# Performance work log

Hardware: AMD Instinct MI355X
Metric: run time of the kernel (lower is better)

Reference implementation:

```python
import jax, jax.numpy as jnp
import numpy as np

CLASS_NUM = 64
CENTROID_MARGIN = 1.4
EPS = 1e-6
N, D = 262144, 128


def setup_inputs() -> dict:
    key = jax.random.key(0)
    k1, k2 = jax.random.split(key)
    embeddings = jax.random.normal(k1, (N, D), dtype=jnp.float32)
    target = jax.random.randint(k2, (N,), 0, CLASS_NUM, dtype=jnp.int32)
    return {"embeddings": embeddings, "target": target}


def reference(embeddings, target):
    C = CLASS_NUM
    dt = embeddings.dtype
    # per-class sums and counts (equivalent to one-hot broadcast-multiply-sum in the original)
    counts = jax.ops.segment_sum(jnp.ones((embeddings.shape[0],), dtype=dt), target, num_segments=C)  # [C]
    sums = jax.ops.segment_sum(embeddings, target, num_segments=C)  # [C, D]
    class_centers = sums / (counts[:, None] + EPS)  # [C, D]
    # pairwise squared distances between centers
    diff = class_centers[:, None, :] - class_centers[None, :, :]  # [C, C, D]
    cc = jnp.sum(diff * diff, axis=2)  # [C, C]
    cc = jax.nn.relu(CENTROID_MARGIN - jnp.sqrt(cc + EPS)) ** 2
    cc = jnp.triu(cc, k=1).sum() / C * (C - 1) / 2
    # L2 distance of each embedding to its class center
    dist = embeddings - class_centers[target]  # [N, D]
    l2 = jnp.sum(dist * dist, axis=1).mean()
    return l2 + cc
```

## Files before the change

kernel.cpp:

```cpp
#include <hip/hip_runtime.h>

#define CLS 64
#define DIM 128
#define NROWS 262144
#define MARGIN 1.4f
#define EPSF 1e-6f
#define FIXSCALE 1048576.0f
#define INVFIX (1.0f / 1048576.0f)
#define SQSCALE 1048576.0
#define INVSQ (1.0 / 1048576.0)
#define NB 256

__global__ __launch_bounds__(256) void zeroK(int* __restrict__ p, int n) {
    int i = blockIdx.x * 256 + threadIdx.x;
    if (i < n) p[i] = 0;
}

__global__ __launch_bounds__(512, 2) void phaseA(const float* __restrict__ emb,
                                                 const int* __restrict__ tgt,
                                                 int* __restrict__ fsum_i,
                                                 int* __restrict__ fcnt_i,
                                                 unsigned long long* __restrict__ sq64,
                                                 int rowsPerBlock) {
    __shared__ int acc[CLS * DIM];
    __shared__ int cnt[CLS];
    __shared__ float red[8];
    const int tid = threadIdx.x;

    for (int i = tid; i < CLS * DIM; i += 512) acc[i] = 0;
    if (tid < CLS) cnt[tid] = 0;
    __syncthreads();

    const int dl = tid & 31;
    const int rl = tid >> 5;
    const int rowBase = blockIdx.x * rowsPerBlock;
    const int iters = rowsPerBlock >> 6;
    int r = rowBase + rl;

    const float4* __restrict__ embv = reinterpret_cast<const float4*>(emb);

    float4 v0 = embv[(size_t)(r)      * 32 + dl];
    float4 v1 = embv[(size_t)(r + 16) * 32 + dl];
    float4 v2 = embv[(size_t)(r + 32) * 32 + dl];
    float4 v3 = embv[(size_t)(r + 48) * 32 + dl];
    int c0 = tgt[r];
    int c1 = tgt[r + 16];
    int c2 = tgt[r + 32];
    int c3 = tgt[r + 48];

    float sq = 0.f;
    for (int it = 0; it < iters; ++it) {
        float4 x0 = v0, x1 = v1, x2 = v2, x3 = v3;
        int k0 = c0, k1 = c1, k2 = c2, k3 = c3;
        int rn = r + 64;
        if (it + 1 < iters) {
            v0 = embv[(size_t)(rn)      * 32 + dl];
            v1 = embv[(size_t)(rn + 16) * 32 + dl];
            v2 = embv[(size_t)(rn + 32) * 32 + dl];
            v3 = embv[(size_t)(rn + 48) * 32 + dl];
            c0 = tgt[rn];
            c1 = tgt[rn + 16];
            c2 = tgt[rn + 32];
            c3 = tgt[rn + 48];
        }
        r = rn;

        sq += x0.x * x0.x + x0.y * x0.y + x0.z * x0.z + x0.w * x0.w;
        sq += x1.x * x1.x + x1.y * x1.y + x1.z * x1.z + x1.w * x1.w;
        sq += x2.x * x2.x + x2.y * x2.y + x2.z * x2.z + x2.w * x2.w;
        sq += x3.x * x3.x + x3.y * x3.y + x3.z * x3.z + x3.w * x3.w;

        int* row0 = &acc[k0 * DIM];
        atomicAdd(&row0[dl],      __float2int_rn(x0.x * FIXSCALE));
        atomicAdd(&row0[32 + dl], __float2int_rn(x0.y * FIXSCALE));
        atomicAdd(&row0[64 + dl], __float2int_rn(x0.z * FIXSCALE));
        atomicAdd(&row0[96 + dl], __float2int_rn(x0.w * FIXSCALE));
        int* row1 = &acc[k1 * DIM];
        atomicAdd(&row1[dl],      __float2int_rn(x1.x * FIXSCALE));
        atomicAdd(&row1[32 + dl], __float2int_rn(x1.y * FIXSCALE));
        atomicAdd(&row1[64 + dl], __float2int_rn(x1.z * FIXSCALE));
        atomicAdd(&row1[96 + dl], __float2int_rn(x1.w * FIXSCALE));
        int* row2 = &acc[k2 * DIM];
        atomicAdd(&row2[dl],      __float2int_rn(x2.x * FIXSCALE));
        atomicAdd(&row2[32 + dl], __float2int_rn(x2.y * FIXSCALE));
        atomicAdd(&row2[64 + dl], __float2int_rn(x2.z * FIXSCALE));
        atomicAdd(&row2[96 + dl], __float2int_rn(x2.w * FIXSCALE));
        int* row3 = &acc[k3 * DIM];
        atomicAdd(&row3[dl],      __float2int_rn(x3.x * FIXSCALE));
        atomicAdd(&row3[32 + dl], __float2int_rn(x3.y * FIXSCALE));
        atomicAdd(&row3[64 + dl], __float2int_rn(x3.z * FIXSCALE));
        atomicAdd(&row3[96 + dl], __float2int_rn(x3.w * FIXSCALE));
        if (dl == 0) {
            atomicAdd(&cnt[k0], 1);
            atomicAdd(&cnt[k1], 1);
            atomicAdd(&cnt[k2], 1);
            atomicAdd(&cnt[k3], 1);
        }
    }

    for (int o = 32; o > 0; o >>= 1) sq += __shfl_down(sq, o, 64);
    if ((tid & 63) == 0) red[tid >> 6] = sq;
    __syncthreads();

    for (int i = tid; i < CLS * DIM; i += 512) atomicAdd(&fsum_i[i], acc[i]);
    if (tid < CLS) atomicAdd(&fcnt_i[tid], cnt[tid]);
    if (tid == 0) {
        double s = 0.0;
        for (int k = 0; k < 8; ++k) s += (double)red[k];
        atomicAdd(sq64, (unsigned long long)(s * SQSCALE + 0.5));
    }
}

__device__ double blockReduceD(double v, double* scratch, int tid) {
    for (int o = 32; o > 0; o >>= 1) v += __shfl_down(v, o, 64);
    if ((tid & 63) == 0) scratch[tid >> 6] = v;
    __syncthreads();
    double t = 0.0;
    if (tid == 0) {
        for (int i = 0; i < 16; ++i) t += scratch[i];
    }
    __syncthreads();
    return t;
}

__global__ __launch_bounds__(1024) void phaseC(const int* __restrict__ fsum_i,
                                               const int* __restrict__ fcnt_i,
                                               const unsigned long long* __restrict__ sq64,
                                               float* __restrict__ out) {
    __shared__ float cenT[DIM][CLS];
    __shared__ float nrm[CLS];
    __shared__ float cInv[CLS];
    __shared__ float cRaw[CLS];
    __shared__ double scratch[16];
    const int tid = threadIdx.x;

    if (tid < CLS) {
        float c = (float)fcnt_i[tid];
        cRaw[tid] = c;
        cInv[tid] = 1.f / (c + EPSF);
    }
    __syncthreads();

    double s1 = 0.0, s2 = 0.0;
    for (int i = tid; i < CLS * DIM; i += 1024) {
        const int c = i >> 7;
        const int d = i & 127;
        float v = (float)fsum_i[i] * INVFIX;
        float ctr = v * cInv[c];
        cenT[d][c] = ctr;
        s1 += (double)(v * ctr);
        s2 += (double)(cRaw[c] * ctr * ctr);
    }
    const double s1t = blockReduceD(s1, scratch, tid);
    const double s2t = blockReduceD(s2, scratch, tid);

    if (tid < CLS) {
        float n = 0.f;
        for (int d = 0; d < DIM; ++d) {
            float v = cenT[d][tid];
            n += v * v;
        }
        nrm[tid] = n;
    }
    __syncthreads();

    const int w = tid >> 6;
    const int b = tid & 63;
    float g0 = 0.f, g1 = 0.f, g2 = 0.f, g3 = 0.f;
    for (int d = 0; d < DIM; ++d) {
        float vb = cenT[d][b];
        g0 += cenT[d][w]      * vb;
        g1 += cenT[d][w + 16] * vb;
        g2 += cenT[d][w + 32] * vb;
        g3 += cenT[d][w + 48] * vb;
    }
    float ccp = 0.f;
    {
        float gs[4] = {g0, g1, g2, g3};
#pragma unroll
        for (int j = 0; j < 4; ++j) {
            const int a = w + 16 * j;
            if (a == b) continue;
            float d2 = nrm[a] + nrm[b] - 2.f * gs[j];
            float val = fmaxf(MARGIN - sqrtf(fmaxf(d2, 0.f) + EPSF), 0.f);
            ccp += val * val;
        }
    }
    const double ccOrd = blockReduceD((double)ccp, scratch, tid);

    if (tid == 0) {
        double triu = ccOrd * 0.5;
        double ccv = triu / 64.0 * 63.0 / 2.0;
        double fsq = (double)sq64[0] * INVSQ;
        double l2 = (fsq - 2.0 * s1t + s2t) / (double)NROWS;
        out[0] = (float)(l2 + ccv);
    }
}

extern "C" void kernel_launch(void* const* d_in, const int* in_sizes, int n_in,
                              void* d_out, int out_size, void* d_ws, size_t ws_size,
                              hipStream_t stream) {
    const float* emb = (const float*)d_in[0];
    const int* tgt = (const int*)d_in[1];
    float* out = (float*)d_out;

    char* ws = (char*)d_ws;
    int* fsum_i = (int*)ws;
    int* fcnt_i = fsum_i + CLS * DIM;
    unsigned long long* sq64 = (unsigned long long*)(ws + 33024);

    const int nZero = CLS * DIM + CLS + 2;
    const int rowsPerBlock = NROWS / NB;

    zeroK<<<(nZero + 255) / 256, 256, 0, stream>>>(fsum_i, nZero);
    phaseA<<<NB, 512, 0, stream>>>(emb, tgt, fsum_i, fcnt_i, sq64, rowsPerBlock);
    phaseC<<<1, 1024, 0, stream>>>(fsum_i, fcnt_i, sq64, out);
}
```

Baseline: 55.40 us.

## Replace global atomics with per-block partials and a separate reduction kernel

Each phaseA block now writes its class sums, counts and squared-norm partial to private workspace slots instead of atomically adding into global fixed-point accumulators, so the zeroing kernel goes away. A new phaseBR kernel reduces the partials across blocks in float and double. The grid also doubles to 512 blocks. This removes global atomic contention and the zero-fill launch. In exchange it writes and rereads about 16 MB of partials and adds another launch, and it changes the summation from fixed-point to float.

```diff
diff --git a/kernel.cpp b/kernel.cpp
--- a/kernel.cpp
+++ b/kernel.cpp
@@ -7,20 +7,13 @@
 #define EPSF 1e-6f
 #define FIXSCALE 1048576.0f
 #define INVFIX (1.0f / 1048576.0f)
-#define SQSCALE 1048576.0
-#define INVSQ (1.0 / 1048576.0)
-#define NB 256
-
-__global__ __launch_bounds__(256) void zeroK(int* __restrict__ p, int n) {
-    int i = blockIdx.x * 256 + threadIdx.x;
-    if (i < n) p[i] = 0;
-}
+#define NB 512
 
 __global__ __launch_bounds__(512, 2) void phaseA(const float* __restrict__ emb,
                                                  const int* __restrict__ tgt,
-                                                 int* __restrict__ fsum_i,
-                                                 int* __restrict__ fcnt_i,
-                                                 unsigned long long* __restrict__ sq64,
+                                                 float* __restrict__ psum,
+                                                 int* __restrict__ pcnt,
+                                                 float* __restrict__ psq,
                                                  int rowsPerBlock) {
     __shared__ int acc[CLS * DIM];
     __shared__ int cnt[CLS];
@@ -102,12 +95,58 @@
     if ((tid & 63) == 0) red[tid >> 6] = sq;
     __syncthreads();
 
-    for (int i = tid; i < CLS * DIM; i += 512) atomicAdd(&fsum_i[i], acc[i]);
-    if (tid < CLS) atomicAdd(&fcnt_i[tid], cnt[tid]);
+    float4* __restrict__ pv = reinterpret_cast<float4*>(psum + (size_t)blockIdx.x * (CLS * DIM));
+    const int4* __restrict__ av = reinterpret_cast<const int4*>(acc);
+    for (int i = tid; i < (CLS * DIM) / 4; i += 512) {
+        int4 a = av[i];
+        pv[i] = make_float4((float)a.x * INVFIX, (float)a.y * INVFIX,
+                            (float)a.z * INVFIX, (float)a.w * INVFIX);
+    }
+    if (tid < CLS) pcnt[blockIdx.x * CLS + tid] = cnt[tid];
     if (tid == 0) {
-        double s = 0.0;
-        for (int k = 0; k < 8; ++k) s += (double)red[k];
-        atomicAdd(sq64, (unsigned long long)(s * SQSCALE + 0.5));
+        float s = 0.f;
+        for (int k = 0; k < 8; ++k) s += red[k];
+        psq[blockIdx.x] = s;
+    }
+}
+
+__global__ __launch_bounds__(256) void phaseBR(const float* __restrict__ psum,
+                                               const int* __restrict__ pcnt,
+                                               const float* __restrict__ psq,
+                                               float* __restrict__ fsum,
+                                               int* __restrict__ fcnt,
+                                               double* __restrict__ fsq) {
+    const int tid = threadIdx.x;
+    if (blockIdx.x < 128) {
+        const int o = blockIdx.x * 64 + (tid & 63);
+        const int q = tid >> 6;
+        const float* __restrict__ p = psum + (size_t)q * 128 * (CLS * DIM) + o;
+        float s0 = 0.f, s1 = 0.f, s2 = 0.f, s3 = 0.f;
+        for (int j = 0; j < 128; j += 4) {
+            s0 += p[(size_t)(j)     * (CLS * DIM)];
+            s1 += p[(size_t)(j + 1) * (CLS * DIM)];
+            s2 += p[(size_t)(j + 2) * (CLS * DIM)];
+            s3 += p[(size_t)(j + 3) * (CLS * DIM)];
+        }
+        __shared__ float sh[4][64];
+        sh[q][tid & 63] = (s0 + s1) + (s2 + s3);
+        __syncthreads();
+        if (tid < 64) fsum[o] = (sh[0][tid] + sh[1][tid]) + (sh[2][tid] + sh[3][tid]);
+    } else {
+        const int c = tid & 63;
+        const int q = tid >> 6;
+        int s = 0;
+        for (int k = q * (NB / 4); k < (q + 1) * (NB / 4); ++k) s += pcnt[k * CLS + c];
+        __shared__ int shc[4][64];
+        shc[q][c] = s;
+        __syncthreads();
+        if (tid < 64) fcnt[tid] = (shc[0][tid] + shc[1][tid]) + (shc[2][tid] + shc[3][tid]);
+        if (tid < 64) {
+            double d = 0.0;
+            for (int k = tid; k < NB; k += 64) d += (double)psq[k];
+            for (int o2 = 32; o2 > 0; o2 >>= 1) d += __shfl_down(d, o2, 64);
+            if (tid == 0) fsq[0] = d;
+        }
     }
 }
 
@@ -123,9 +162,9 @@
     return t;
 }
 
-__global__ __launch_bounds__(1024) void phaseC(const int* __restrict__ fsum_i,
-                                               const int* __restrict__ fcnt_i,
-                                               const unsigned long long* __restrict__ sq64,
+__global__ __launch_bounds__(1024) void phaseC(const float* __restrict__ fsum,
+                                               const int* __restrict__ fcnt,
+                                               const double* __restrict__ fsq,
                                                float* __restrict__ out) {
     __shared__ float cenT[DIM][CLS];
     __shared__ float nrm[CLS];
@@ -135,7 +174,7 @@
     const int tid = threadIdx.x;
 
     if (tid < CLS) {
-        float c = (float)fcnt_i[tid];
+        float c = (float)fcnt[tid];
         cRaw[tid] = c;
         cInv[tid] = 1.f / (c + EPSF);
     }
@@ -145,7 +184,7 @@
     for (int i = tid; i < CLS * DIM; i += 1024) {
         const int c = i >> 7;
         const int d = i & 127;
-        float v = (float)fsum_i[i] * INVFIX;
+        float v = fsum[i];
         float ctr = v * cInv[c];
         cenT[d][c] = ctr;
         s1 += (double)(v * ctr);
@@ -191,8 +230,7 @@
     if (tid == 0) {
         double triu = ccOrd * 0.5;
         double ccv = triu / 64.0 * 63.0 / 2.0;
-        double fsq = (double)sq64[0] * INVSQ;
-        double l2 = (fsq - 2.0 * s1t + s2t) / (double)NROWS;
+        double l2 = (fsq[0] - 2.0 * s1t + s2t) / (double)NROWS;
         out[0] = (float)(l2 + ccv);
     }
 }
@@ -205,14 +243,16 @@
     float* out = (float*)d_out;
 
     char* ws = (char*)d_ws;
-    int* fsum_i = (int*)ws;
-    int* fcnt_i = fsum_i + CLS * DIM;
-    unsigned long long* sq64 = (unsigned long long*)(ws + 33024);
-
-    const int nZero = CLS * DIM + CLS + 2;
+    float* fsum = (float*)ws;
+    int* fcnt = (int*)(ws + 32768);
+    double* fsq = (double*)(ws + 33024);
+    float* psum = (float*)(ws + 65536);
+    int* pcnt = (int*)(ws + 65536 + (size_t)NB * CLS * DIM * 4);
+    float* psq = (float*)(ws + 65536 + (size_t)NB * CLS * DIM * 4 + (size_t)NB * CLS * 4);
+
     const int rowsPerBlock = NROWS / NB;
 
-    zeroK<<<(nZero + 255) / 256, 256, 0, stream>>>(fsum_i, nZero);
-    phaseA<<<NB, 512, 0, stream>>>(emb, tgt, fsum_i, fcnt_i, sq64, rowsPerBlock);
-    phaseC<<<1, 1024, 0, stream>>>(fsum_i, fcnt_i, sq64, out);
-}
+    phaseA<<<NB, 512, 0, stream>>>(emb, tgt, psum, pcnt, psq, rowsPerBlock);
+    phaseBR<<<129, 256, 0, stream>>>(psum, pcnt, psq, fsum, fcnt, fsq);
+    phaseC<<<1, 1024, 0, stream>>>(fsum, fcnt, fsq, out);
+}
```

New measurement: 55.38 us. Within noise of the previous version (-0.0%).
